# Optimization experiments

Measured on AMD Instinct MI355X. Metric: run time of the kernel, lower is better.

Reference implementation:

```python
import jax, jax.numpy as jnp
import numpy as np

DIM = 1024
NUM_HEADS = 16
WINDOW_SIZE = 512
HEAD_DIM = DIM // NUM_HEADS
SCALE = HEAD_DIM ** (-0.5)


def setup_inputs() -> dict:
    key = jax.random.key(0)
    kq, kk, kv = jax.random.split(key, 3)
    shape = (2, NUM_HEADS, 2048, HEAD_DIM)
    q = jax.random.normal(kq, shape, dtype=jnp.float32)
    k = jax.random.normal(kk, shape, dtype=jnp.float32)
    v = jax.random.normal(kv, shape, dtype=jnp.float32)
    return {"q": q, "k": k, "v": v}


def reference(q, k, v):
    B, H, N, D = q.shape
    pos = jnp.arange(N)
    # causal + sliding window: col <= row and col >= row - w + 1
    window_mask = (pos[None, :] <= pos[:, None]) & (pos[None, :] >= pos[:, None] - WINDOW_SIZE + 1)  # (N, N)
    attn = jnp.einsum("bhnd,bhmd->bhnm", q, k) * SCALE  # (B, H, N, N)
    attn = jnp.where(window_mask[None, None], attn, -jnp.inf)
    attn = jax.nn.softmax(attn, axis=-1)
    attn = jnp.nan_to_num(attn, nan=0.0)
    return jnp.einsum("bhnm,bhmd->bhnd", attn, v)
```

## Files before the change

### kernel.cpp

```cpp
#include <hip/hip_runtime.h>
#include <math.h>


#define SEQ 2048
#define HD  64
#define BM  64
#define BN  64
#define LDR 72

typedef short short8 __attribute__((ext_vector_type(8)));
typedef float f32x4  __attribute__((ext_vector_type(4)));

static __device__ inline unsigned short f2bf(float f){
  union{float f; unsigned u;} un; un.f=f;
  return (unsigned short)((un.u + 0x7FFFu + ((un.u>>16)&1u))>>16);
}

__global__ __launch_bounds__(256) void swa_fwd(
    const float* __restrict__ q, const float* __restrict__ k,
    const float* __restrict__ v, float* __restrict__ out)
{
  __shared__ short Qs[BM*LDR];
  __shared__ short Ps[BM*LDR];
  __shared__ short Ks[2][BN*LDR];
  __shared__ short Vt[2][HD*LDR];

  const int tid=threadIdx.x, bid=blockIdx.x;
  const int mtile=bid&31, bh=bid>>5, m0=mtile*BM;
  const long base=(long)bh*SEQ*HD;
  const int wv=tid>>6, lane=tid&63, quad=lane>>4, l16=lane&15;
  const int dcol=lane;

  {
    const float4* qg=(const float4*)(q+base+(long)m0*HD);
    #pragma unroll
    for(int i=0;i<4;++i){
      int idx=i*256+tid, r=idx>>4, c4=idx&15;
      float4 f=qg[idx];
      ushort4 h; h.x=f2bf(f.x); h.y=f2bf(f.y); h.z=f2bf(f.z); h.w=f2bf(f.w);
      *(ushort4*)&Qs[r*LDR+c4*4]=h;
    }
  }

  const int tb=mtile, tlo=(tb>8)?(tb-8):0;

  float4 kreg[4];
  float  vcol[4][4];
  {
    const float4* kg=(const float4*)(k+base+(long)(tlo*BN)*HD);
    const float*  vg=v+base+(long)(tlo*BN)*HD;
    #pragma unroll
    for(int i=0;i<4;++i) kreg[i]=kg[i*256+tid];
    #pragma unroll
    for(int g=0;g<4;++g){
      int r0=wv*4+g*16;
      #pragma unroll
      for(int j=0;j<4;++j) vcol[g][j]=vg[(r0+j)*HD+dcol];
    }
  }
  __syncthreads();

  short8 qa[2];
  #pragma unroll
  for(int kk=0;kk<2;++kk)
    qa[kk]=*(const short8*)&Qs[(wv*16+l16)*LDR+kk*32+quad*8];

  {
    #pragma unroll
    for(int i=0;i<4;++i){
      int idx=i*256+tid, r=idx>>4, c4=idx&15;
      float4 fk=kreg[i];
      ushort4 hk; hk.x=f2bf(fk.x); hk.y=f2bf(fk.y); hk.z=f2bf(fk.z); hk.w=f2bf(fk.w);
      *(ushort4*)&Ks[0][r*LDR+c4*4]=hk;
    }
    #pragma unroll
    for(int g=0;g<4;++g){
      int r0=wv*4+g*16;
      ushort4 hv; hv.x=f2bf(vcol[g][0]); hv.y=f2bf(vcol[g][1]);
                  hv.z=f2bf(vcol[g][2]); hv.w=f2bf(vcol[g][3]);
      *(ushort4*)&Vt[0][dcol*LDR+r0]=hv;
    }
  }

  float lrun[4]={0.f,0.f,0.f,0.f};
  f32x4 oacc[4];
  #pragma unroll
  for(int dt=0;dt<4;++dt) oacc[dt]=(f32x4){0.f,0.f,0.f,0.f};

  __syncthreads();

  for(int t=tlo;t<=tb;++t){
    const int buf=(t-tlo)&1;
    const int j0=t*BN;

    f32x4 sacc[4];
    #pragma unroll
    for(int nt=0;nt<4;++nt) sacc[nt]=(f32x4){0.f,0.f,0.f,0.f};
    #pragma unroll
    for(int kk=0;kk<2;++kk){
      #pragma unroll
      for(int nt=0;nt<4;++nt){
        short8 kb=*(const short8*)&Ks[buf][(nt*16+l16)*LDR+kk*32+quad*8];
        sacc[nt]=__builtin_amdgcn_mfma_f32_16x16x32_bf16(qa[kk],kb,sacc[nt],0,0,0);
      }
    }

    if(t<tb){
      const float4* kg=(const float4*)(k+base+(long)((t+1)*BN)*HD);
      const float*  vg=v+base+(long)((t+1)*BN)*HD;
      #pragma unroll
      for(int i=0;i<4;++i) kreg[i]=kg[i*256+tid];
      #pragma unroll
      for(int g=0;g<4;++g){
        int r0=wv*4+g*16;
        #pragma unroll
        for(int j=0;j<4;++j) vcol[g][j]=vg[(r0+j)*HD+dcol];
      }
    }

    #pragma unroll
    for(int r=0;r<4;++r){
      const int grr=m0+wv*16+quad*4+r;
      #pragma unroll
      for(int nt=0;nt<4;++nt){
        const int gc=j0+nt*16+l16;
        float e=exp2f(sacc[nt][r]*0.18033688011112042f);
        float p=((gc<=grr)&&(gc>=grr-511))?e:0.f;
        lrun[r]+=p;
        Ps[(wv*16+quad*4+r)*LDR+nt*16+l16]=(short)f2bf(p);
      }
    }
    __syncthreads();

    #pragma unroll
    for(int kk=0;kk<2;++kk){
      short8 pa=*(const short8*)&Ps[(wv*16+l16)*LDR+kk*32+quad*8];
      #pragma unroll
      for(int dt=0;dt<4;++dt){
        short8 vb=*(const short8*)&Vt[buf][(dt*16+l16)*LDR+kk*32+quad*8];
        oacc[dt]=__builtin_amdgcn_mfma_f32_16x16x32_bf16(pa,vb,oacc[dt],0,0,0);
      }
    }

    if(t<tb){
      #pragma unroll
      for(int i=0;i<4;++i){
        int idx=i*256+tid, r=idx>>4, c4=idx&15;
        float4 fk=kreg[i];
        ushort4 hk; hk.x=f2bf(fk.x); hk.y=f2bf(fk.y); hk.z=f2bf(fk.z); hk.w=f2bf(fk.w);
        *(ushort4*)&Ks[buf^1][r*LDR+c4*4]=hk;
      }
      #pragma unroll
      for(int g=0;g<4;++g){
        int r0=wv*4+g*16;
        ushort4 hv; hv.x=f2bf(vcol[g][0]); hv.y=f2bf(vcol[g][1]);
                    hv.z=f2bf(vcol[g][2]); hv.w=f2bf(vcol[g][3]);
        *(ushort4*)&Vt[buf^1][dcol*LDR+r0]=hv;
      }
    }
    __syncthreads();
  }

  #pragma unroll
  for(int r=0;r<4;++r){
    float s=lrun[r];
    s+=__shfl_xor(s,1); s+=__shfl_xor(s,2); s+=__shfl_xor(s,4); s+=__shfl_xor(s,8);
    lrun[r]=(s>0.f)?(1.f/s):0.f;
  }
  #pragma unroll
  for(int r=0;r<4;++r){
    const int row=m0+wv*16+quad*4+r;
    #pragma unroll
    for(int dt=0;dt<4;++dt)
      out[base+(long)row*HD+dt*16+l16]=oacc[dt][r]*lrun[r];
  }
}

extern "C" void kernel_launch(void* const* d_in, const int* in_sizes, int n_in,
                              void* d_out, int out_size, void* d_ws, size_t ws_size,
                              hipStream_t stream) {
  const float* q=(const float*)d_in[0];
  const float* k=(const float*)d_in[1];
  const float* v=(const float*)d_in[2];
  float* o=(float*)d_out;
  dim3 grid(32*32);
  dim3 block(256);
  hipLaunchKernelGGL(swa_fwd, grid, block, 0, stream, q, k, v, o);
}
```

Before: 127.6 us.

## Rewrite sliding-window attention with 128-row tiles, register-resident P and swizzled LDS

Each block now covers 128 query rows with 8 waves (512 threads) instead of 64 rows with 4 waves, so every staged K/V tile is shared by twice as many query rows and total global K/V traffic drops. S is computed transposed (K as the A operand), which lets the exponentiated probabilities be packed straight into registers as the PV MFMA operand. This removes the P round-trip through shared memory and one barrier per iteration. Q is pre-scaled, the mask runs only on boundary tiles, exp uses the hardware builtin, P is truncated rather than rounded to bf16, and XOR-swizzled LDS layouts replace the padding. The costs are half the number of blocks and idle waves on tiles that fall outside a wave's window.

```diff
diff --git a/kernel.cpp b/kernel.cpp
--- a/kernel.cpp
+++ b/kernel.cpp
@@ -1,189 +1,195 @@
 #include <hip/hip_runtime.h>
-#include <math.h>
 
 
 #define SEQ 2048
 #define HD  64
-#define BM  64
-#define BN  64
-#define LDR 72
 
 typedef short short8 __attribute__((ext_vector_type(8)));
 typedef float f32x4  __attribute__((ext_vector_type(4)));
+typedef int   i32x4  __attribute__((ext_vector_type(4)));
 
 static __device__ inline unsigned short f2bf(float f){
   union{float f; unsigned u;} un; un.f=f;
   return (unsigned short)((un.u + 0x7FFFu + ((un.u>>16)&1u))>>16);
 }
+static __device__ inline int swz(int row){ return (row&3)|(((row>>3)&1)<<2); }
 
-__global__ __launch_bounds__(256) void swa_fwd(
+__global__ __launch_bounds__(512) void swa_fused(
     const float* __restrict__ q, const float* __restrict__ k,
     const float* __restrict__ v, float* __restrict__ out)
 {
-  __shared__ short Qs[BM*LDR];
-  __shared__ short Ps[BM*LDR];
-  __shared__ short Ks[2][BN*LDR];
-  __shared__ short Vt[2][HD*LDR];
+  __shared__ unsigned short Ks[2][4096];
+  __shared__ unsigned short Vsh[2][4096];
 
   const int tid=threadIdx.x, bid=blockIdx.x;
-  const int mtile=bid&31, bh=bid>>5, m0=mtile*BM;
+  const int mt=bid&15, bh=bid>>4, m0=mt*128;
   const long base=(long)bh*SEQ*HD;
   const int wv=tid>>6, lane=tid&63, quad=lane>>4, l16=lane&15;
-  const int dcol=lane;
+  const int qrow=m0+wv*16+l16;
+  const int h=wv>>2;
 
+  short8 qa[2];
   {
-    const float4* qg=(const float4*)(q+base+(long)m0*HD);
+    const float C=0.18033688011112042f;
+    const float* qp=q+base+(long)qrow*HD+quad*8;
     #pragma unroll
-    for(int i=0;i<4;++i){
-      int idx=i*256+tid, r=idx>>4, c4=idx&15;
-      float4 f=qg[idx];
-      ushort4 h; h.x=f2bf(f.x); h.y=f2bf(f.y); h.z=f2bf(f.z); h.w=f2bf(f.w);
-      *(ushort4*)&Qs[r*LDR+c4*4]=h;
+    for(int kk=0;kk<2;++kk){
+      float4 f0=*(const float4*)(qp+kk*32);
+      float4 f1=*(const float4*)(qp+kk*32+4);
+      short8 a;
+      a[0]=(short)f2bf(f0.x*C); a[1]=(short)f2bf(f0.y*C);
+      a[2]=(short)f2bf(f0.z*C); a[3]=(short)f2bf(f0.w*C);
+      a[4]=(short)f2bf(f1.x*C); a[5]=(short)f2bf(f1.y*C);
+      a[6]=(short)f2bf(f1.z*C); a[7]=(short)f2bf(f1.w*C);
+      qa[kk]=a;
     }
   }
 
-  const int tb=mtile, tlo=(tb>8)?(tb-8):0;
+  const int rbase=8*(l16>>2)+(l16&3);
+  const int swk=(l16&3)|(((l16>>2)&1)<<2);
+  const int swv=(l16&3)|(((l16>>3)&1)<<2);
+  int kaoff[2][4], vboff[2][4];
+  #pragma unroll
+  for(int kk=0;kk<2;++kk){
+    #pragma unroll
+    for(int nt=0;nt<4;++nt)
+      kaoff[kk][nt]=(rbase+(nt&1)*4+(nt>>1)*32)*64+(((quad+4*kk)^swk)*8);
+    #pragma unroll
+    for(int dt=0;dt<4;++dt)
+      vboff[kk][dt]=(dt*16+l16)*64+(((quad+4*kk)^swv)*8);
+  }
 
-  float4 kreg[4];
-  float  vcol[4][4];
+  const int kr=tid>>3, klc=tid&7;
+  const int kwaddr=kr*64+((klc^swz(kr))*8);
+  const int vw=tid>>6, vd=tid&63;
+  const int vwaddr=vd*64+((vw^swz(vd))*8);
+  const float* kg=k+base;
+  const float* vg=v+base;
+
+  f32x4 oacc[4];
+  #pragma unroll
+  for(int dt=0;dt<4;++dt) oacc[dt]=(f32x4){0.f,0.f,0.f,0.f};
+  float lrun=0.f;
+
+  const int Tb =2*mt+1;
+  const int Tlo=(2*mt>8)?(2*mt-8):0;
+  const int myTb=2*mt+h;
+  const bool clip=(myTb>=8);
+  const int myTlo=clip?(myTb-8):0;
+
   {
-    const float4* kg=(const float4*)(k+base+(long)(tlo*BN)*HD);
-    const float*  vg=v+base+(long)(tlo*BN)*HD;
+    const float* kt=kg+(long)Tlo*4096;
+    const float* vt=vg+(long)Tlo*4096;
+    float4 kf0=*(const float4*)(kt+kr*64+klc*8);
+    float4 kf1=*(const float4*)(kt+kr*64+klc*8+4);
+    float vf[8];
     #pragma unroll
-    for(int i=0;i<4;++i) kreg[i]=kg[i*256+tid];
+    for(int j=0;j<8;++j) vf[j]=vt[(vw*8+j)*64+vd];
+    unsigned short hk[8];
+    hk[0]=f2bf(kf0.x); hk[1]=f2bf(kf0.y); hk[2]=f2bf(kf0.z); hk[3]=f2bf(kf0.w);
+    hk[4]=f2bf(kf1.x); hk[5]=f2bf(kf1.y); hk[6]=f2bf(kf1.z); hk[7]=f2bf(kf1.w);
+    *(uint4*)&Ks[0][kwaddr]=*(uint4*)hk;
+    unsigned short hv[8];
     #pragma unroll
-    for(int g=0;g<4;++g){
-      int r0=wv*4+g*16;
-      #pragma unroll
-      for(int j=0;j<4;++j) vcol[g][j]=vg[(r0+j)*HD+dcol];
-    }
+    for(int j=0;j<8;++j) hv[j]=f2bf(vf[j]);
+    *(uint4*)&Vsh[0][vwaddr]=*(uint4*)hv;
   }
   __syncthreads();
 
-  short8 qa[2];
-  #pragma unroll
-  for(int kk=0;kk<2;++kk)
-    qa[kk]=*(const short8*)&Qs[(wv*16+l16)*LDR+kk*32+quad*8];
+  for(int t=Tlo;t<=Tb;++t){
+    const int buf=(t-Tlo)&1;
+    const bool pf=(t<Tb);
 
-  {
-    #pragma unroll
-    for(int i=0;i<4;++i){
-      int idx=i*256+tid, r=idx>>4, c4=idx&15;
-      float4 fk=kreg[i];
-      ushort4 hk; hk.x=f2bf(fk.x); hk.y=f2bf(fk.y); hk.z=f2bf(fk.z); hk.w=f2bf(fk.w);
-      *(ushort4*)&Ks[0][r*LDR+c4*4]=hk;
+    float4 kf0,kf1; float vf[8];
+    if(pf){
+      const float* kt=kg+(long)(t+1)*4096;
+      const float* vt=vg+(long)(t+1)*4096;
+      kf0=*(const float4*)(kt+kr*64+klc*8);
+      kf1=*(const float4*)(kt+kr*64+klc*8+4);
+      #pragma unroll
+      for(int j=0;j<8;++j) vf[j]=vt[(vw*8+j)*64+vd];
     }
-    #pragma unroll
-    for(int g=0;g<4;++g){
-      int r0=wv*4+g*16;
-      ushort4 hv; hv.x=f2bf(vcol[g][0]); hv.y=f2bf(vcol[g][1]);
-                  hv.z=f2bf(vcol[g][2]); hv.w=f2bf(vcol[g][3]);
-      *(ushort4*)&Vt[0][dcol*LDR+r0]=hv;
-    }
-  }
 
-  float lrun[4]={0.f,0.f,0.f,0.f};
-  f32x4 oacc[4];
-  #pragma unroll
-  for(int dt=0;dt<4;++dt) oacc[dt]=(f32x4){0.f,0.f,0.f,0.f};
+    if(t>=myTlo && t<=myTb){
+      f32x4 sacc[4];
+      #pragma unroll
+      for(int nt=0;nt<4;++nt) sacc[nt]=(f32x4){0.f,0.f,0.f,0.f};
+      #pragma unroll
+      for(int kk=0;kk<2;++kk)
+        #pragma unroll
+        for(int nt=0;nt<4;++nt){
+          short8 ka=*(const short8*)&Ks[buf][kaoff[kk][nt]];
+          sacc[nt]=__builtin_amdgcn_mfma_f32_16x16x32_bf16(ka,qa[kk],sacc[nt],0,0,0);
+        }
 
-  __syncthreads();
-
-  for(int t=tlo;t<=tb;++t){
-    const int buf=(t-tlo)&1;
-    const int j0=t*BN;
-
-    f32x4 sacc[4];
-    #pragma unroll
-    for(int nt=0;nt<4;++nt) sacc[nt]=(f32x4){0.f,0.f,0.f,0.f};
-    #pragma unroll
-    for(int kk=0;kk<2;++kk){
+      unsigned pp[8];
+      float ls=0.f;
+      const bool msk=(t==myTb)||(clip&&t==myTlo);
       #pragma unroll
       for(int nt=0;nt<4;++nt){
-        short8 kb=*(const short8*)&Ks[buf][(nt*16+l16)*LDR+kk*32+quad*8];
-        sacc[nt]=__builtin_amdgcn_mfma_f32_16x16x32_bf16(qa[kk],kb,sacc[nt],0,0,0);
+        float e0=__builtin_amdgcn_exp2f(sacc[nt][0]);
+        float e1=__builtin_amdgcn_exp2f(sacc[nt][1]);
+        float e2=__builtin_amdgcn_exp2f(sacc[nt][2]);
+        float e3=__builtin_amdgcn_exp2f(sacc[nt][3]);
+        if(msk){
+          const int kb0=t*64+8*quad+(nt&1)*4+(nt>>1)*32;
+          e0=((kb0+0<=qrow)&&(kb0+0+511>=qrow))?e0:0.f;
+          e1=((kb0+1<=qrow)&&(kb0+1+511>=qrow))?e1:0.f;
+          e2=((kb0+2<=qrow)&&(kb0+2+511>=qrow))?e2:0.f;
+          e3=((kb0+3<=qrow)&&(kb0+3+511>=qrow))?e3:0.f;
+        }
+        ls+=e0+e1+e2+e3;
+        pp[nt*2+0]=(__float_as_uint(e1)&0xFFFF0000u)|(__float_as_uint(e0)>>16);
+        pp[nt*2+1]=(__float_as_uint(e3)&0xFFFF0000u)|(__float_as_uint(e2)>>16);
+      }
+      lrun+=ls;
+      i32x4 i0={(int)pp[0],(int)pp[1],(int)pp[2],(int)pp[3]};
+      i32x4 i1={(int)pp[4],(int)pp[5],(int)pp[6],(int)pp[7]};
+      short8 pa0=*(short8*)&i0;
+      short8 pa1=*(short8*)&i1;
+
+      #pragma unroll
+      for(int dt=0;dt<4;++dt){
+        short8 vb0=*(const short8*)&Vsh[buf][vboff[0][dt]];
+        short8 vb1=*(const short8*)&Vsh[buf][vboff[1][dt]];
+        oacc[dt]=__builtin_amdgcn_mfma_f32_16x16x32_bf16(pa0,vb0,oacc[dt],0,0,0);
+        oacc[dt]=__builtin_amdgcn_mfma_f32_16x16x32_bf16(pa1,vb1,oacc[dt],0,0,0);
       }
     }
 
-    if(t<tb){
-      const float4* kg=(const float4*)(k+base+(long)((t+1)*BN)*HD);
-      const float*  vg=v+base+(long)((t+1)*BN)*HD;
+    if(pf){
+      unsigned short hk[8];
+      hk[0]=f2bf(kf0.x); hk[1]=f2bf(kf0.y); hk[2]=f2bf(kf0.z); hk[3]=f2bf(kf0.w);
+      hk[4]=f2bf(kf1.x); hk[5]=f2bf(kf1.y); hk[6]=f2bf(kf1.z); hk[7]=f2bf(kf1.w);
+      *(uint4*)&Ks[buf^1][kwaddr]=*(uint4*)hk;
+      unsigned short hv[8];
       #pragma unroll
-      for(int i=0;i<4;++i) kreg[i]=kg[i*256+tid];
-      #pragma unroll
-      for(int g=0;g<4;++g){
-        int r0=wv*4+g*16;
-        #pragma unroll
-        for(int j=0;j<4;++j) vcol[g][j]=vg[(r0+j)*HD+dcol];
-      }
-    }
-
-    #pragma unroll
-    for(int r=0;r<4;++r){
-      const int grr=m0+wv*16+quad*4+r;
-      #pragma unroll
-      for(int nt=0;nt<4;++nt){
-        const int gc=j0+nt*16+l16;
-        float e=exp2f(sacc[nt][r]*0.18033688011112042f);
-        float p=((gc<=grr)&&(gc>=grr-511))?e:0.f;
-        lrun[r]+=p;
-        Ps[(wv*16+quad*4+r)*LDR+nt*16+l16]=(short)f2bf(p);
-      }
-    }
-    __syncthreads();
-
-    #pragma unroll
-    for(int kk=0;kk<2;++kk){
-      short8 pa=*(const short8*)&Ps[(wv*16+l16)*LDR+kk*32+quad*8];
-      #pragma unroll
-      for(int dt=0;dt<4;++dt){
-        short8 vb=*(const short8*)&Vt[buf][(dt*16+l16)*LDR+kk*32+quad*8];
-        oacc[dt]=__builtin_amdgcn_mfma_f32_16x16x32_bf16(pa,vb,oacc[dt],0,0,0);
-      }
-    }
-
-    if(t<tb){
-      #pragma unroll
-      for(int i=0;i<4;++i){
-        int idx=i*256+tid, r=idx>>4, c4=idx&15;
-        float4 fk=kreg[i];
-        ushort4 hk; hk.x=f2bf(fk.x); hk.y=f2bf(fk.y); hk.z=f2bf(fk.z); hk.w=f2bf(fk.w);
-        *(ushort4*)&Ks[buf^1][r*LDR+c4*4]=hk;
-      }
-      #pragma unroll
-      for(int g=0;g<4;++g){
-        int r0=wv*4+g*16;
-        ushort4 hv; hv.x=f2bf(vcol[g][0]); hv.y=f2bf(vcol[g][1]);
-                    hv.z=f2bf(vcol[g][2]); hv.w=f2bf(vcol[g][3]);
-        *(ushort4*)&Vt[buf^1][dcol*LDR+r0]=hv;
-      }
+      for(int j=0;j<8;++j) hv[j]=f2bf(vf[j]);
+      *(uint4*)&Vsh[buf^1][vwaddr]=*(uint4*)hv;
     }
     __syncthreads();
   }
 
+  lrun+=__shfl_xor(lrun,16);
+  lrun+=__shfl_xor(lrun,32);
+  float linv=1.0f/lrun;
   #pragma unroll
   for(int r=0;r<4;++r){
-    float s=lrun[r];
-    s+=__shfl_xor(s,1); s+=__shfl_xor(s,2); s+=__shfl_xor(s,4); s+=__shfl_xor(s,8);
-    lrun[r]=(s>0.f)?(1.f/s):0.f;
-  }
-  #pragma unroll
-  for(int r=0;r<4;++r){
-    const int row=m0+wv*16+quad*4+r;
+    float lr=__shfl(linv,quad*4+r);
+    const int orow=m0+wv*16+quad*4+r;
     #pragma unroll
     for(int dt=0;dt<4;++dt)
-      out[base+(long)row*HD+dt*16+l16]=oacc[dt][r]*lrun[r];
+      out[base+(long)orow*HD+dt*16+l16]=oacc[dt][r]*lr;
   }
 }
 
 extern "C" void kernel_launch(void* const* d_in, const int* in_sizes, int n_in,
                               void* d_out, int out_size, void* d_ws, size_t ws_size,
                               hipStream_t stream) {
+  (void)in_sizes; (void)n_in; (void)out_size; (void)d_ws; (void)ws_size;
   const float* q=(const float*)d_in[0];
   const float* k=(const float*)d_in[1];
   const float* v=(const float*)d_in[2];
   float* o=(float*)d_out;
-  dim3 grid(32*32);
-  dim3 block(256);
-  hipLaunchKernelGGL(swa_fwd, grid, block, 0, stream, q, k, v, o);
+  hipLaunchKernelGGL(swa_fused, dim3(512), dim3(512), 0, stream, q, k, v, o);
 }
```

After: 108.2 us. 15.2% less time.
